# Performance work log

Measured on AMD Instinct MI355X. Metric: run time of the kernel, lower is better.

The kernel has to match this reference:

```python
import jax, jax.numpy as jnp
import numpy as np

N, K, M, C, OUT, S = 80000, 8, 1000, 128, 64, 2
EPS = 1e-5


def _bn(x, g, b, m, v):
    # eval-mode BatchNorm1d applied over the last (channel) axis
    return (x - m) * (g / jnp.sqrt(v + EPS)) + b


def setup_inputs() -> dict:
    key = jax.random.key(0)
    ks = jax.random.split(key, 40)
    it = iter(range(40))
    rn = lambda sh, s=1.0: jax.random.normal(ks[next(it)], sh, dtype=jnp.float32) * s
    ru = lambda sh: jax.random.uniform(ks[next(it)], sh, dtype=jnp.float32, minval=0.5, maxval=1.5)
    w = 0.05
    inp = {}
    inp["sp_fea"] = rn((M, C))
    inp["sp_xyz"] = rn((M, 3))
    inp["o_p_fea"] = rn((N, C))
    inp["p_xyz"] = rn((N, 3))
    # linear_q / linear_k / linear_v  (in_planes -> mid_planes)
    inp["Wq"] = rn((C, C), w); inp["bq"] = jnp.zeros((C,), jnp.float32)
    inp["Wk"] = rn((C, C), w); inp["bk"] = jnp.zeros((C,), jnp.float32)
    inp["Wv"] = rn((C, C), w); inp["bv"] = jnp.zeros((C,), jnp.float32)
    # linear_p: Linear(3,3) -> BN(3) -> ReLU -> Linear(3, mid)
    inp["Wp1"] = rn((3, 3), 0.5); inp["bp1"] = jnp.zeros((3,), jnp.float32)
    inp["gp"] = 1.0 + rn((3,), 0.1); inp["betap"] = rn((3,), 0.1)
    inp["mp"] = rn((3,), 0.1); inp["vp"] = ru((3,))
    inp["Wp2"] = rn((3, C), 0.3); inp["bp2"] = jnp.zeros((C,), jnp.float32)
    # linear_w: BN(mid) -> ReLU -> Linear(mid,out) -> BN(out) -> ReLU -> Linear(out,out)
    inp["g1"] = 1.0 + rn((C,), 0.1); inp["beta1"] = rn((C,), 0.1)
    inp["m1"] = rn((C,), 0.1); inp["v1"] = ru((C,))
    inp["W1"] = rn((C, OUT), w); inp["b1"] = jnp.zeros((OUT,), jnp.float32)
    inp["g2"] = 1.0 + rn((OUT,), 0.1); inp["beta2"] = rn((OUT,), 0.1)
    inp["m2"] = rn((OUT,), 0.1); inp["v2"] = ru((OUT,))
    inp["W2"] = rn((OUT, OUT), w); inp["b2"] = jnp.zeros((OUT,), jnp.float32)
    # index / offset inputs (ints)
    inp["c2p_idx_abs"] = jax.random.randint(ks[next(it)], (N, K), 0, M)
    inp["c2p_idx"] = jax.random.randint(ks[next(it)], (N, K), 0, M)
    inp["cluster_idx"] = jax.random.randint(ks[next(it)], (N,), 0, M)
    inp["offset"] = jnp.array([N], dtype=jnp.int32)
    inp["sp_offset"] = jnp.array([M], dtype=jnp.int32)
    return inp


def reference(sp_fea, sp_xyz, o_p_fea, p_xyz,
              Wq, bq, Wk, bk, Wv, bv,
              Wp1, bp1, gp, betap, mp, vp, Wp2, bp2,
              g1, beta1, m1, v1, W1, b1,
              g2, beta2, m2, v2, W2, b2,
              c2p_idx_abs, c2p_idx, cluster_idx, offset, sp_offset):
    q = o_p_fea @ Wq + bq                               # [N, C]
    k_sp = (sp_fea @ Wk + bk)[c2p_idx_abs]              # gather -> [N, K, C]
    v_sp = (sp_fea @ Wv + bv)[c2p_idx_abs]              # [N, K, C]
    p_e = sp_xyz[c2p_idx_abs]                           # [N, K, 3]
    # positional encoding MLP
    p_e = jax.nn.relu(_bn(p_e @ Wp1 + bp1, gp, betap, mp, vp)) @ Wp2 + bp2  # [N, K, C]
    # vector attention scores
    w = k_sp - q[:, None, :] + p_e                      # [N, K, C]
    w = jax.nn.relu(_bn(w, g1, beta1, m1, v1)) @ W1 + b1
    w = jax.nn.relu(_bn(w, g2, beta2, m2, v2)) @ W2 + b2  # [N, K, OUT]
    w = jax.nn.softmax(w, axis=1)                        # softmax over the K neighbors
    # shared-plane weighted sum
    bi = ((v_sp + p_e).reshape(N, K, S, C // S) * w[:, :, None, :]).reshape(N, K, C)
    bi = bi.sum(axis=2)                                  # [N, K]
    return jax.nn.softmax(bi, axis=1)                    # association matrix [N, K]
```

## Files before the change

kernel.cpp:

```cpp
#include <hip/hip_runtime.h>
#include <stdint.h>

#define EPS 1e-5f
#define LOG2E 1.4426950408889634f

#define NPTS 80000
#define CDIM 128
#define ODIM 64
#define KNBR 8
#define MSUP 1000

#define KP2H_OFF 0
#define UT_OFF   (256*1024)
#define WQF_OFF  (512*1024)
#define W1F_OFF  (544*1024)
#define W2F_OFF  (560*1024)
#define C1_OFF   (568*1024)
#define QSG_OFF  (576*1024)
#define WSTAGE_BYTES (16*1024 + 8*1024 + 256)

typedef float f32x4 __attribute__((ext_vector_type(4)));
typedef short bf16x8 __attribute__((ext_vector_type(8)));
typedef __bf16 bf16v8 __attribute__((ext_vector_type(8)));
typedef __bf16 bf16v4 __attribute__((ext_vector_type(4)));

union FragU { bf16x8 v; unsigned u[4]; uint4 q; };

#if __has_builtin(__builtin_amdgcn_cvt_pk_bf16_f32)
#define HAVE_PK_BF16 1
#endif

__device__ inline unsigned pk_bf16(float lo, float hi) {
#ifdef HAVE_PK_BF16
  typedef __bf16 bf16x2_t __attribute__((ext_vector_type(2)));
  return __builtin_bit_cast(unsigned, __builtin_amdgcn_cvt_pk_bf16_f32(lo, hi));
#else
  unsigned a = __builtin_bit_cast(unsigned, lo);
  unsigned b = __builtin_bit_cast(unsigned, hi);
  a += 0x7FFFu + ((a >> 16) & 1u);
  b += 0x7FFFu + ((b >> 16) & 1u);
  return (a >> 16) | (b & 0xFFFF0000u);
#endif
}

__device__ inline float exp2_fast(float x) {
#if __has_builtin(__builtin_amdgcn_exp2f)
  return __builtin_amdgcn_exp2f(x);
#else
  return exp2f(x);
#endif
}

__global__ __launch_bounds__(256)
void k_prep(const float* __restrict__ sp_fea, const float* __restrict__ sp_xyz,
            const float* __restrict__ Wk, const float* __restrict__ bk,
            const float* __restrict__ Wv, const float* __restrict__ bv,
            const float* __restrict__ Wp1, const float* __restrict__ bp1,
            const float* __restrict__ gp, const float* __restrict__ betap,
            const float* __restrict__ mp, const float* __restrict__ vp,
            const float* __restrict__ Wp2, const float* __restrict__ bp2,
            const float* __restrict__ g1, const float* __restrict__ beta1,
            const float* __restrict__ m1, const float* __restrict__ v1,
            const float* __restrict__ bq,
            const float* __restrict__ Wq, const float* __restrict__ W1,
            const float* __restrict__ W2,
            const float* __restrict__ g2, const float* __restrict__ v2,
            const float* __restrict__ b1, const float* __restrict__ m2,
            const float* __restrict__ beta2, char* __restrict__ ws)
{
  if (blockIdx.x < 1000) {
    unsigned short* kp2h = (unsigned short*)(ws + KP2H_OFF);
    float* uT = (float*)(ws + UT_OFF);
    const int m = blockIdx.x;
    const int t = threadIdx.x;
    const int c = t & 127, half = t >> 7;
    __shared__ float fea[128];
    __shared__ float pk[128], pv[128];
    if (t < 128) fea[t] = sp_fea[m * 128 + t];
    __syncthreads();
    float kv = 0.f, vv = 0.f;
    const float* wkc = Wk + half * 64 * 128 + c;
    const float* wvc = Wv + half * 64 * 128 + c;
    const float* feah = fea + half * 64;
    #pragma unroll 8
    for (int d = 0; d < 64; ++d) {
      const float f = feah[d];
      kv = fmaf(f, wkc[d * 128], kv);
      vv = fmaf(f, wvc[d * 128], vv);
    }
    if (half) { pk[c] = kv; pv[c] = vv; }
    __syncthreads();
    if (!half) {
      kv += pk[c] + bk[c];
      vv += pv[c] + bv[c];
      const float x0 = sp_xyz[m*3+0], x1 = sp_xyz[m*3+1], x2 = sp_xyz[m*3+2];
      float pe = bp2[c];
      #pragma unroll
      for (int ii = 0; ii < 3; ++ii) {
        float s = bp1[ii] + x0*Wp1[0*3+ii] + x1*Wp1[1*3+ii] + x2*Wp1[2*3+ii];
        s = (s - mp[ii]) * (gp[ii] * rsqrtf(vp[ii] + EPS)) + betap[ii];
        s = fmaxf(s, 0.0f);
        pe += s * Wp2[ii*128 + c];
      }
      const float s1c = g1[c] * rsqrtf(v1[c] + EPS);
      const float kpv = (kv + pe - m1[c] - bq[c]) * s1c + beta1[c];
      kp2h[m*128 + c] = (unsigned short)(pk_bf16(kpv, kpv) & 0xFFFFu);
      pv[c] = vv + pe;
    }
    __syncthreads();
    if (t < 64) {
      const int j = (t >> 2) + (t & 3) * 16;
      uT[m*64 + t] = (pv[j] + pv[j + 64]) * LOG2E;
    }
  } else {
    const int tid = (blockIdx.x - 1000) * 256 + threadIdx.x;
    if (tid < 2048) {
      const int e = tid, f = e >> 6, l = e & 63;
      const int kt = f >> 3, mt = f & 7;
      const int c = mt*16 + (l & 15);
      const int d0 = kt*32 + (l >> 4)*8;
      const float sc = g1[c] * rsqrtf(v1[c] + EPS);
      uint4 u;
      u.x = pk_bf16(Wq[(d0+0)*128 + c]*sc, Wq[(d0+1)*128 + c]*sc);
      u.y = pk_bf16(Wq[(d0+2)*128 + c]*sc, Wq[(d0+3)*128 + c]*sc);
      u.z = pk_bf16(Wq[(d0+4)*128 + c]*sc, Wq[(d0+5)*128 + c]*sc);
      u.w = pk_bf16(Wq[(d0+6)*128 + c]*sc, Wq[(d0+7)*128 + c]*sc);
      *(uint4*)(ws + WQF_OFF + e*16) = u;
    } else if (tid < 3072) {
      const int e = tid - 2048, f = e >> 6, l = e & 63;
      const int kt = f >> 2, jt = f & 3;
      const int j = jt*16 + (l & 15);
      const int c0 = kt*32 + (l >> 4)*8;
      const float sc = g2[j] * rsqrtf(v2[j] + EPS);
      uint4 u;
      u.x = pk_bf16(W1[(c0+0)*64 + j]*sc, W1[(c0+1)*64 + j]*sc);
      u.y = pk_bf16(W1[(c0+2)*64 + j]*sc, W1[(c0+3)*64 + j]*sc);
      u.z = pk_bf16(W1[(c0+4)*64 + j]*sc, W1[(c0+5)*64 + j]*sc);
      u.w = pk_bf16(W1[(c0+6)*64 + j]*sc, W1[(c0+7)*64 + j]*sc);
      *(uint4*)(ws + W1F_OFF + e*16) = u;
    } else if (tid < 3584) {
      const int e = tid - 3072, f = e >> 6, l = e & 63;
      const int kt2 = f >> 2, nt = f & 3;
      const int jp = nt*16 + (l & 15);
      const int j0 = kt2*32 + (l >> 4)*8;
      uint4 u;
      u.x = pk_bf16(W2[(j0+0)*64 + jp]*LOG2E, W2[(j0+1)*64 + jp]*LOG2E);
      u.y = pk_bf16(W2[(j0+2)*64 + jp]*LOG2E, W2[(j0+3)*64 + jp]*LOG2E);
      u.z = pk_bf16(W2[(j0+4)*64 + jp]*LOG2E, W2[(j0+5)*64 + jp]*LOG2E);
      u.w = pk_bf16(W2[(j0+6)*64 + jp]*LOG2E, W2[(j0+7)*64 + jp]*LOG2E);
      *(uint4*)(ws + W2F_OFF + e*16) = u;
    } else if (tid < 3648) {
      const int j = tid - 3584;
      const float sc = g2[j] * rsqrtf(v2[j] + EPS);
      ((float*)(ws + C1_OFF))[j] = (b1[j] - m2[j]) * sc + beta2[j];
    }
  }
}

__global__ __launch_bounds__(256, 4)
void k_q(const float* __restrict__ o_p_fea, char* __restrict__ ws)
{
  __shared__ __align__(16) char ldsq[32*1024];
  char* qs_g = ws + QSG_OFF;
  const int t = threadIdx.x;
  const int wave = t >> 6, l = t & 63;
  const int quad = l >> 4, row = l & 15;
  const int n0 = (blockIdx.x * 4 + wave) * 16;

  {
    const uint4* src = (const uint4*)(ws + WQF_OFF);
    uint4* dst = (uint4*)ldsq;
    #pragma unroll
    for (int i = 0; i < 8; ++i) dst[t + i*256] = src[t + i*256];
  }
  __syncthreads();

  f32x4 qa[8];
  #pragma unroll
  for (int mt = 0; mt < 8; ++mt) qa[mt] = (f32x4){0.f, 0.f, 0.f, 0.f};
  const float* feab = o_p_fea + (size_t)(n0 + row) * 128;
  #pragma unroll
  for (int kt = 0; kt < 4; ++kt) {
    f32x4 fa = *(const f32x4*)(feab + kt*32 + quad*8);
    f32x4 fb = *(const f32x4*)(feab + kt*32 + quad*8 + 4);
    FragU bu;
    bu.u[0] = pk_bf16(fa[0], fa[1]);
    bu.u[1] = pk_bf16(fa[2], fa[3]);
    bu.u[2] = pk_bf16(fb[0], fb[1]);
    bu.u[3] = pk_bf16(fb[2], fb[3]);
    #pragma unroll
    for (int mt = 0; mt < 8; ++mt) {
      const bf16x8 wf = *(const bf16x8*)(ldsq + ((kt*8+mt)*64 + l)*16);
      qa[mt] = __builtin_amdgcn_mfma_f32_16x16x32_bf16(wf, bu.v, qa[mt], 0, 0, 0);
    }
  }
  #pragma unroll
  for (int mt = 0; mt < 8; ++mt) {
    uint2 pp;
    pp.x = pk_bf16(qa[mt][0], qa[mt][1]);
    pp.y = pk_bf16(qa[mt][2], qa[mt][3]);
    *(uint2*)(qs_g + (size_t)(n0 + row) * 256 + mt*32 + quad*8) = pp;
  }
}

#define H2_PITCH 144
#define H2_SIZE  (16*144)
#define W1L_OFF  0
#define W2L_OFF  (16*1024)
#define C1L_OFF  (24*1024)
#define H2_BASE  24832
#define LDS_TOTAL (H2_BASE + 4*H2_SIZE)

__global__ __launch_bounds__(256, 3)
void k_main(const int* __restrict__ idx, const float* __restrict__ b2,
            const char* __restrict__ ws, float* __restrict__ out)
{
  const unsigned short* kp2h = (const unsigned short*)(ws + KP2H_OFF);
  const float* uT = (const float*)(ws + UT_OFF);
  const char* qs_g = ws + QSG_OFF;

  __shared__ __align__(16) char lds[LDS_TOTAL];
  const int t = threadIdx.x;
  const int wave = t >> 6, l = t & 63;
  const int quad = l >> 4, row = l & 15;
  char* h2_w = lds + H2_BASE + wave * H2_SIZE;

  const int slot = blockIdx.x * 4 + wave;
  const int gid0 = slot * 4;
  const int nloc = row >> 3;

  {
    const uint4* src = (const uint4*)(ws + W1F_OFF);
    uint4* dst = (uint4*)lds;
    #pragma unroll
    for (int i = 0; i < 7; ++i) {
      const int e = t + i * 256;
      if (e < WSTAGE_BYTES / 16) dst[e] = src[e];
    }
  }

  int mr4[4];
  #pragma unroll
  for (int g = 0; g < 4; ++g) mr4[g] = idx[(gid0 + g)*16 + row];

  __syncthreads();

  f32x4 c1r[4];
  #pragma unroll
  for (int jt = 0; jt < 4; ++jt)
    c1r[jt] = *(const f32x4*)(lds + C1L_OFF + (jt*16 + quad*4)*4);
  float b2r[4];
  #pragma unroll
  for (int nt = 0; nt < 4; ++nt) b2r[nt] = b2[row + nt*16] * LOG2E;

  int msc[4];
  #pragma unroll
  for (int rg = 0; rg < 4; ++rg) msc[rg] = idx[gid0*16 + quad*4 + rg];
  uint4 kfc[4], qpc[4];
  {
    const uint4* kr = (const uint4*)(kp2h + (size_t)mr4[0] * 128);
    const uint4* qr = (const uint4*)(qs_g + (size_t)(gid0*2 + nloc) * 256);
    #pragma unroll
    for (int kt = 0; kt < 4; ++kt) { kfc[kt] = kr[kt*4 + quad]; qpc[kt] = qr[kt*4 + quad]; }
  }

  #pragma unroll 1
  for (int g = 0; g < 4; ++g) {
    const int gid = gid0 + g;
    int msn[4];
    uint4 kfn[4], qpn[4];
    if (g < 3) {
      #pragma unroll
      for (int rg = 0; rg < 4; ++rg) msn[rg] = idx[(gid+1)*16 + quad*4 + rg];
      const uint4* kr = (const uint4*)(kp2h + (size_t)mr4[g+1] * 128);
      const uint4* qr = (const uint4*)(qs_g + (size_t)((gid+1)*2 + nloc) * 256);
      #pragma unroll
      for (int kt = 0; kt < 4; ++kt) { kfn[kt] = kr[kt*4 + quad]; qpn[kt] = qr[kt*4 + quad]; }
    }
    f32x4 u4[4];
    #pragma unroll
    for (int rg = 0; rg < 4; ++rg)
      u4[rg] = *(const f32x4*)(uT + (size_t)msc[rg] * 64 + row * 4);

    f32x4 a1[4];
    #pragma unroll
    for (int jt = 0; jt < 4; ++jt) a1[jt] = (f32x4){0.f, 0.f, 0.f, 0.f};
    #pragma unroll
    for (int kt = 0; kt < 4; ++kt) {
      const bf16v8 kv = __builtin_bit_cast(bf16v8, kfc[kt]);
      const bf16v8 qv = __builtin_bit_cast(bf16v8, qpc[kt]);
      bf16v8 z = {};
      bf16v8 x = __builtin_elementwise_max((bf16v8)(kv - qv), z);
      FragU xf;
      xf.q = __builtin_bit_cast(uint4, x);
      #pragma unroll
      for (int jt = 0; jt < 4; ++jt) {
        const bf16x8 wf = *(const bf16x8*)(lds + W1L_OFF + (kt*4+jt)*1024 + l*16);
        a1[jt] = __builtin_amdgcn_mfma_f32_16x16x32_bf16(wf, xf.v, a1[jt], 0, 0, 0);
      }
    }

    #pragma unroll
    for (int jt = 0; jt < 4; ++jt) {
      f32x4 v = a1[jt] + c1r[jt];
      uint2 pp;
      pp.x = pk_bf16(v[0], v[1]);
      pp.y = pk_bf16(v[2], v[3]);
      bf16v4 h = __builtin_bit_cast(bf16v4, pp);
      bf16v4 z4 = {};
      h = __builtin_elementwise_max(h, z4);
      pp = __builtin_bit_cast(uint2, h);
      *(uint2*)(h2_w + row*H2_PITCH + (jt*16 + quad*4)*2) = pp;
    }

    f32x4 a2[4];
    #pragma unroll
    for (int nt = 0; nt < 4; ++nt) a2[nt] = (f32x4){0.f, 0.f, 0.f, 0.f};
    #pragma unroll
    for (int kt2 = 0; kt2 < 2; ++kt2) {
      const bf16x8 af = *(const bf16x8*)(h2_w + row*H2_PITCH + kt2*64 + quad*16);
      #pragma unroll
      for (int nt = 0; nt < 4; ++nt) {
        const bf16x8 wf = *(const bf16x8*)(lds + W2L_OFF + (kt2*4+nt)*1024 + l*16);
        a2[nt] = __builtin_amdgcn_mfma_f32_16x16x32_bf16(af, wf, a2[nt], 0, 0, 0);
      }
    }
    float e[4][4], rs[4];
    #pragma unroll
    for (int nt = 0; nt < 4; ++nt) {
      #pragma unroll
      for (int rg = 0; rg < 4; ++rg) e[nt][rg] = exp2_fast(a2[nt][rg] + b2r[nt]);
      float s = e[nt][0] + e[nt][1] + e[nt][2] + e[nt][3];
      s += __shfl_xor(s, 16);
      rs[nt] = __builtin_amdgcn_rcpf(s);
    }
    float bi[4] = {0.f, 0.f, 0.f, 0.f};
    #pragma unroll
    for (int rg = 0; rg < 4; ++rg) {
      #pragma unroll
      for (int nt = 0; nt < 4; ++nt)
        bi[rg] = fmaf(e[nt][rg] * rs[nt], u4[rg][nt], bi[rg]);
    }
    #pragma unroll
    for (int rg = 0; rg < 4; ++rg) {
      float b = bi[rg];
      b += __shfl_xor(b, 1);
      b += __shfl_xor(b, 2);
      b += __shfl_xor(b, 4);
      b += __shfl_xor(b, 8);
      bi[rg] = b;
    }
    const float eb0 = exp2_fast(bi[0]), eb1 = exp2_fast(bi[1]);
    const float eb2 = exp2_fast(bi[2]), eb3 = exp2_fast(bi[3]);
    float sb = eb0 + eb1 + eb2 + eb3;
    sb += __shfl_xor(sb, 16);
    const float rsb = __builtin_amdgcn_rcpf(sb);
    if (row < 4) {
      const float vsel = row == 0 ? eb0 : row == 1 ? eb1 : row == 2 ? eb2 : eb3;
      out[gid*16 + quad*4 + row] = vsel * rsb;
    }
    if (g < 3) {
      #pragma unroll
      for (int rg = 0; rg < 4; ++rg) msc[rg] = msn[rg];
      #pragma unroll
      for (int kt = 0; kt < 4; ++kt) { kfc[kt] = kfn[kt]; qpc[kt] = qpn[kt]; }
    }
  }
}

extern "C" void kernel_launch(void* const* d_in, const int* in_sizes, int n_in,
                              void* d_out, int out_size, void* d_ws, size_t ws_size,
                              hipStream_t stream)
{
  const float* sp_fea  = (const float*)d_in[0];
  const float* sp_xyz  = (const float*)d_in[1];
  const float* o_p_fea = (const float*)d_in[2];
  const float* Wq    = (const float*)d_in[4];
  const float* bq    = (const float*)d_in[5];
  const float* Wk    = (const float*)d_in[6];
  const float* bk    = (const float*)d_in[7];
  const float* Wv    = (const float*)d_in[8];
  const float* bv    = (const float*)d_in[9];
  const float* Wp1   = (const float*)d_in[10];
  const float* bp1   = (const float*)d_in[11];
  const float* gp    = (const float*)d_in[12];
  const float* betap = (const float*)d_in[13];
  const float* mp    = (const float*)d_in[14];
  const float* vp    = (const float*)d_in[15];
  const float* Wp2   = (const float*)d_in[16];
  const float* bp2   = (const float*)d_in[17];
  const float* g1    = (const float*)d_in[18];
  const float* beta1 = (const float*)d_in[19];
  const float* m1    = (const float*)d_in[20];
  const float* v1    = (const float*)d_in[21];
  const float* W1    = (const float*)d_in[22];
  const float* b1    = (const float*)d_in[23];
  const float* g2    = (const float*)d_in[24];
  const float* beta2 = (const float*)d_in[25];
  const float* m2    = (const float*)d_in[26];
  const float* v2    = (const float*)d_in[27];
  const float* W2    = (const float*)d_in[28];
  const float* b2    = (const float*)d_in[29];
  const int* c2p_idx_abs = (const int*)d_in[30];

  char* ws = (char*)d_ws;
  float* out = (float*)d_out;

  hipLaunchKernelGGL(k_prep, dim3(1015), dim3(256), 0, stream,
                     sp_fea, sp_xyz, Wk, bk, Wv, bv, Wp1, bp1, gp, betap, mp, vp,
                     Wp2, bp2, g1, beta1, m1, v1, bq,
                     Wq, W1, W2, g2, v2, b1, m2, beta2, ws);
  hipLaunchKernelGGL(k_q, dim3(1250), dim3(256), 0, stream,
                     o_p_fea, ws);
  hipLaunchKernelGGL(k_main, dim3(2500), dim3(256), 0, stream,
                     c2p_idx_abs, b2, ws, out);
}
```

Measured before the change: 213.1 us.

## Fuse q projection into main kernel and keep q tile in LDS

Removes the separate k_q kernel. Each k_main block now computes the bf16 q projection for its 32 points with MFMA, reading Wq fragments straight from global memory, and stores the result in a padded LDS tile. The main loop then reads q from LDS instead of from a global workspace buffer. This saves one kernel launch and the write and re-read of the q intermediate. In exchange, LDS per block grows, the Wq fragments are fetched from global or L2 by every block, and the prologue before the main loop gets longer.

```diff
diff --git a/kernel.cpp b/kernel.cpp
--- a/kernel.cpp
+++ b/kernel.cpp
@@ -16,7 +16,6 @@
 #define W1F_OFF  (544*1024)
 #define W2F_OFF  (560*1024)
 #define C1_OFF   (568*1024)
-#define QSG_OFF  (576*1024)
 #define WSTAGE_BYTES (16*1024 + 8*1024 + 256)
 
 typedef float f32x4 __attribute__((ext_vector_type(4)));
@@ -157,67 +156,23 @@
   }
 }
 
-__global__ __launch_bounds__(256, 4)
-void k_q(const float* __restrict__ o_p_fea, char* __restrict__ ws)
-{
-  __shared__ __align__(16) char ldsq[32*1024];
-  char* qs_g = ws + QSG_OFF;
-  const int t = threadIdx.x;
-  const int wave = t >> 6, l = t & 63;
-  const int quad = l >> 4, row = l & 15;
-  const int n0 = (blockIdx.x * 4 + wave) * 16;
-
-  {
-    const uint4* src = (const uint4*)(ws + WQF_OFF);
-    uint4* dst = (uint4*)ldsq;
-    #pragma unroll
-    for (int i = 0; i < 8; ++i) dst[t + i*256] = src[t + i*256];
-  }
-  __syncthreads();
-
-  f32x4 qa[8];
-  #pragma unroll
-  for (int mt = 0; mt < 8; ++mt) qa[mt] = (f32x4){0.f, 0.f, 0.f, 0.f};
-  const float* feab = o_p_fea + (size_t)(n0 + row) * 128;
-  #pragma unroll
-  for (int kt = 0; kt < 4; ++kt) {
-    f32x4 fa = *(const f32x4*)(feab + kt*32 + quad*8);
-    f32x4 fb = *(const f32x4*)(feab + kt*32 + quad*8 + 4);
-    FragU bu;
-    bu.u[0] = pk_bf16(fa[0], fa[1]);
-    bu.u[1] = pk_bf16(fa[2], fa[3]);
-    bu.u[2] = pk_bf16(fb[0], fb[1]);
-    bu.u[3] = pk_bf16(fb[2], fb[3]);
-    #pragma unroll
-    for (int mt = 0; mt < 8; ++mt) {
-      const bf16x8 wf = *(const bf16x8*)(ldsq + ((kt*8+mt)*64 + l)*16);
-      qa[mt] = __builtin_amdgcn_mfma_f32_16x16x32_bf16(wf, bu.v, qa[mt], 0, 0, 0);
-    }
-  }
-  #pragma unroll
-  for (int mt = 0; mt < 8; ++mt) {
-    uint2 pp;
-    pp.x = pk_bf16(qa[mt][0], qa[mt][1]);
-    pp.y = pk_bf16(qa[mt][2], qa[mt][3]);
-    *(uint2*)(qs_g + (size_t)(n0 + row) * 256 + mt*32 + quad*8) = pp;
-  }
-}
-
 #define H2_PITCH 144
 #define H2_SIZE  (16*144)
 #define W1L_OFF  0
 #define W2L_OFF  (16*1024)
 #define C1L_OFF  (24*1024)
 #define H2_BASE  24832
-#define LDS_TOTAL (H2_BASE + 4*H2_SIZE)
+#define QL_OFF   (H2_BASE + 4*H2_SIZE)
+#define QL_PITCH 272
+#define LDS_TOTAL (QL_OFF + 32*QL_PITCH)
 
 __global__ __launch_bounds__(256, 3)
 void k_main(const int* __restrict__ idx, const float* __restrict__ b2,
+            const float* __restrict__ o_p_fea,
             const char* __restrict__ ws, float* __restrict__ out)
 {
   const unsigned short* kp2h = (const unsigned short*)(ws + KP2H_OFF);
   const float* uT = (const float*)(ws + UT_OFF);
-  const char* qs_g = ws + QSG_OFF;
 
   __shared__ __align__(16) char lds[LDS_TOTAL];
   const int t = threadIdx.x;
@@ -236,6 +191,43 @@
     for (int i = 0; i < 7; ++i) {
       const int e = t + i * 256;
       if (e < WSTAGE_BYTES / 16) dst[e] = src[e];
+    }
+  }
+
+  {
+    const int tile = wave >> 1;
+    const int mt0 = (wave & 1) * 4;
+    const int nq = blockIdx.x * 32 + tile * 16 + row;
+    const float* feab = o_p_fea + (size_t)nq * 128;
+    FragU bu[4];
+    #pragma unroll
+    for (int kt = 0; kt < 4; ++kt) {
+      f32x4 fa = *(const f32x4*)(feab + kt*32 + quad*8);
+      f32x4 fb = *(const f32x4*)(feab + kt*32 + quad*8 + 4);
+      bu[kt].u[0] = pk_bf16(fa[0], fa[1]);
+      bu[kt].u[1] = pk_bf16(fa[2], fa[3]);
+      bu[kt].u[2] = pk_bf16(fb[0], fb[1]);
+      bu[kt].u[3] = pk_bf16(fb[2], fb[3]);
+    }
+    f32x4 qa[4];
+    #pragma unroll
+    for (int mt = 0; mt < 4; ++mt) qa[mt] = (f32x4){0.f, 0.f, 0.f, 0.f};
+    #pragma unroll
+    for (int mt = 0; mt < 4; ++mt) {
+      #pragma unroll
+      for (int kt = 0; kt < 4; ++kt) {
+        FragU wf;
+        wf.q = *(const uint4*)(ws + WQF_OFF + (((kt*8 + mt0 + mt)*64 + l) * 16));
+        qa[mt] = __builtin_amdgcn_mfma_f32_16x16x32_bf16(wf.v, bu[kt].v, qa[mt], 0, 0, 0);
+      }
+    }
+    char* lq = lds + QL_OFF + (tile*16 + row) * QL_PITCH;
+    #pragma unroll
+    for (int mt = 0; mt < 4; ++mt) {
+      uint2 pp;
+      pp.x = pk_bf16(qa[mt][0], qa[mt][1]);
+      pp.y = pk_bf16(qa[mt][2], qa[mt][3]);
+      *(uint2*)(lq + (mt0 + mt)*32 + quad*8) = pp;
     }
   }
 
@@ -256,31 +248,37 @@
   int msc[4];
   #pragma unroll
   for (int rg = 0; rg < 4; ++rg) msc[rg] = idx[gid0*16 + quad*4 + rg];
-  uint4 kfc[4], qpc[4];
+  uint4 kfc[4];
   {
     const uint4* kr = (const uint4*)(kp2h + (size_t)mr4[0] * 128);
-    const uint4* qr = (const uint4*)(qs_g + (size_t)(gid0*2 + nloc) * 256);
-    #pragma unroll
-    for (int kt = 0; kt < 4; ++kt) { kfc[kt] = kr[kt*4 + quad]; qpc[kt] = qr[kt*4 + quad]; }
+    #pragma unroll
+    for (int kt = 0; kt < 4; ++kt) kfc[kt] = kr[kt*4 + quad];
   }
 
   #pragma unroll 1
   for (int g = 0; g < 4; ++g) {
     const int gid = gid0 + g;
     int msn[4];
-    uint4 kfn[4], qpn[4];
+    uint4 kfn[4];
     if (g < 3) {
       #pragma unroll
       for (int rg = 0; rg < 4; ++rg) msn[rg] = idx[(gid+1)*16 + quad*4 + rg];
       const uint4* kr = (const uint4*)(kp2h + (size_t)mr4[g+1] * 128);
-      const uint4* qr = (const uint4*)(qs_g + (size_t)((gid+1)*2 + nloc) * 256);
-      #pragma unroll
-      for (int kt = 0; kt < 4; ++kt) { kfn[kt] = kr[kt*4 + quad]; qpn[kt] = qr[kt*4 + quad]; }
+      #pragma unroll
+      for (int kt = 0; kt < 4; ++kt) kfn[kt] = kr[kt*4 + quad];
     }
     f32x4 u4[4];
     #pragma unroll
     for (int rg = 0; rg < 4; ++rg)
       u4[rg] = *(const f32x4*)(uT + (size_t)msc[rg] * 64 + row * 4);
+
+    uint4 qpc[4];
+    {
+      const char* lqr = lds + QL_OFF + (wave*8 + g*2 + nloc) * QL_PITCH;
+      #pragma unroll
+      for (int kt = 0; kt < 4; ++kt)
+        qpc[kt] = *(const uint4*)(lqr + (kt*4 + quad)*16);
+    }
 
     f32x4 a1[4];
     #pragma unroll
@@ -363,7 +361,7 @@
       #pragma unroll
       for (int rg = 0; rg < 4; ++rg) msc[rg] = msn[rg];
       #pragma unroll
-      for (int kt = 0; kt < 4; ++kt) { kfc[kt] = kfn[kt]; qpc[kt] = qpn[kt]; }
+      for (int kt = 0; kt < 4; ++kt) kfc[kt] = kfn[kt];
     }
   }
 }
@@ -410,8 +408,6 @@
                      sp_fea, sp_xyz, Wk, bk, Wv, bv, Wp1, bp1, gp, betap, mp, vp,
                      Wp2, bp2, g1, beta1, m1, v1, bq,
                      Wq, W1, W2, g2, v2, b1, m2, beta2, ws);
-  hipLaunchKernelGGL(k_q, dim3(1250), dim3(256), 0, stream,
-                     o_p_fea, ws);
   hipLaunchKernelGGL(k_main, dim3(2500), dim3(256), 0, stream,
-                     c2p_idx_abs, b2, ws, out);
+                     c2p_idx_abs, b2, o_p_fea, ws, out);
 }
```

Measured after the change: 207.1 us. 2.8% less time.
